# Performance work log

Measured on AMD Instinct MI355X. Metric: run time of the kernel, lower is better.

## Reference

```python
import jax, jax.numpy as jnp
import numpy as np

N_HEAD = 4
D_K = 64
D_V = 64
D_MODEL = 256
LN_EPS = 1e-5


def setup_inputs() -> dict:
    key = jax.random.key(0)
    k1, k2, k3 = jax.random.split(key, 3)
    B, C, H, W = 2, D_MODEL, 64, 64
    q = jax.random.normal(k1, (B, C, H, W), dtype=jnp.float32)
    # w_qkvs: Linear(d_model, n_head*d_k, bias=False), weight [out, in]
    std_qkv = np.sqrt(2.0 / (D_MODEL + D_K))
    w_qkv = jax.random.normal(k2, (N_HEAD * D_K, D_MODEL), dtype=jnp.float32) * std_qkv
    # fc: Linear(n_head*d_v, d_model), xavier-normal-ish init
    std_fc = np.sqrt(2.0 / (N_HEAD * D_V + D_MODEL))
    fc_w = jax.random.normal(k3, (D_MODEL, N_HEAD * D_V), dtype=jnp.float32) * std_fc
    fc_b = jnp.zeros((D_MODEL,), dtype=jnp.float32)
    ln_g = jnp.ones((D_MODEL,), dtype=jnp.float32)
    ln_b = jnp.zeros((D_MODEL,), dtype=jnp.float32)
    return {"q": q, "w_qkv": w_qkv, "fc_w": fc_w, "fc_b": fc_b, "ln_g": ln_g, "ln_b": ln_b}


def reference(q, w_qkv, fc_w, fc_b, ln_g, ln_b):
    B, C, H, W = q.shape
    L = H * W
    # [B, C, H, W] -> [B, L, C]
    x = q.reshape(B, C, L).transpose(0, 2, 1)
    residual = x
    # shared QKV projection (self-attention branch: q == k == v)
    qkv = x @ w_qkv.T                                  # [B, L, nh*dk]
    qh = qkv.reshape(B, L, N_HEAD, D_K).transpose(2, 0, 1, 3)  # [h, B, L, dk]
    scale = jnp.asarray(np.sqrt(D_K), dtype=q.dtype)
    attn = jnp.einsum('hbqd,hbkd->hbqk', qh, qh) / scale       # [h, B, L, L]
    attn = jax.nn.softmax(attn, axis=-1)
    out = jnp.einsum('hbqk,hbkd->hbqd', attn, qh)              # [h, B, L, dv]
    # [h, B, L, dv] -> [B, L, h*dv]
    out = out.transpose(1, 2, 0, 3).reshape(B, L, N_HEAD * D_V)
    out = out @ fc_w.T + fc_b
    out = out + residual
    mu = jnp.mean(out, axis=-1, keepdims=True)
    var = jnp.mean(jnp.square(out - mu), axis=-1, keepdims=True)
    out = (out - mu) / jnp.sqrt(var + LN_EPS) * ln_g + ln_b
    # raw row-major view back to [B, C, H, W] (matches torch .view)
    return out.reshape(B, -1, H, W)
```

## Files before the change

kernel.cpp:

```cpp
#include <hip/hip_runtime.h>

#define L_SEQ 4096
#define DMODEL 256
#define DH 64
#define NKB 16

typedef __attribute__((ext_vector_type(8))) __bf16 bf16x8;
typedef __attribute__((ext_vector_type(4))) float f32x4;
typedef __attribute__((ext_vector_type(16))) float f32x16;
typedef __attribute__((ext_vector_type(8))) unsigned short ushort8v;
typedef __attribute__((ext_vector_type(4))) unsigned short ushort4v;
typedef __attribute__((ext_vector_type(2))) unsigned int uint2v;
typedef __attribute__((ext_vector_type(4))) unsigned int uint4v;

__device__ __forceinline__ unsigned short f2bf(float f) {
  unsigned u = __builtin_bit_cast(unsigned, f);
  u += 0x7fffu + ((u >> 16) & 1u);
  return (unsigned short)(u >> 16);
}
__device__ __forceinline__ float bf2f(unsigned short h) {
  unsigned u = ((unsigned)h) << 16;
  return __builtin_bit_cast(float, u);
}
__device__ __forceinline__ bf16x8 ld_frag(const unsigned short* p) {
  return __builtin_bit_cast(bf16x8, *(const ushort8v*)p);
}
__device__ __forceinline__ unsigned cvtpk(float lo, float hi) {
  unsigned r;
  asm("v_cvt_pk_bf16_f32 %0, %1, %2" : "=v"(r) : "v"(lo), "v"(hi));
  return r;
}
__device__ __forceinline__ void plswap(unsigned& a, unsigned& b) {
  asm("v_permlane32_swap_b32 %0, %1" : "+v"(a), "+v"(b));
}

__global__ __launch_bounds__(256) void k_transpose(const float* __restrict__ q,
                                                   unsigned short* __restrict__ xbf,
                                                   const float* __restrict__ w,
                                                   const float* __restrict__ fcw,
                                                   unsigned short* __restrict__ wbf,
                                                   unsigned short* __restrict__ fcwbf) {
  int bx = blockIdx.x;
  int t = threadIdx.x;
  if (bx >= 512) {
    int i = ((bx - 512) * 256 + t) * 4;
    float4 a = *(const float4*)(w + i);
    float4 b = *(const float4*)(fcw + i);
    ushort4v av = {f2bf(a.x), f2bf(a.y), f2bf(a.z), f2bf(a.w)};
    ushort4v bv = {f2bf(b.x), f2bf(b.y), f2bf(b.z), f2bf(b.w)};
    *(ushort4v*)(wbf + i) = av;
    *(ushort4v*)(fcwbf + i) = bv;
    return;
  }
  __shared__ float T[64 * 65];
  int b = bx >> 8, rest = bx & 255;
  int ct = rest >> 6, lt = rest & 63;
#pragma unroll
  for (int it = 0; it < 4; ++it) {
    int i = (t >> 4) + it * 16;
    int j0 = (t & 15) * 4;
    float4 v = *(const float4*)(q + ((size_t)(b * 256 + ct * 64 + i)) * 4096 + lt * 64 + j0);
    T[i * 65 + j0 + 0] = v.x;
    T[i * 65 + j0 + 1] = v.y;
    T[i * 65 + j0 + 2] = v.z;
    T[i * 65 + j0 + 3] = v.w;
  }
  __syncthreads();
#pragma unroll
  for (int it = 0; it < 2; ++it) {
    int l = (t >> 3) + it * 32;
    int c0 = (t & 7) * 8;
    ushort8v o;
#pragma unroll
    for (int k = 0; k < 8; ++k) o[k] = f2bf(T[(c0 + k) * 65 + l]);
    *(ushort8v*)(xbf + ((size_t)(b * 4096 + lt * 64 + l)) * 256 + ct * 64 + c0) = o;
  }
}

#define KP2 136
__global__ __launch_bounds__(256) void k_qkv(const unsigned short* __restrict__ xbf,
                                             const unsigned short* __restrict__ wbf,
                                             unsigned short* __restrict__ Qh,
                                             unsigned short* __restrict__ QhT) {
  __shared__ unsigned short As[64 * KP2];
  __shared__ unsigned short Bs[64 * KP2];
  int bx = blockIdx.x;
  int mtile = bx >> 2, h = bx & 3;
  int m0 = mtile * 64;
  int b = m0 >> 12, l0 = m0 & 4095;
  int t = threadIdx.x;
  int wv = t >> 6, lane = t & 63, g = lane >> 4, ln = lane & 15;
  f32x4 acc[4] = {};
  for (int kb = 0; kb < 2; ++kb) {
#pragma unroll
    for (int it = 0; it < 4; ++it) {
      int idx = t + it * 256;
      int row = idx >> 4;
      int c0 = (idx & 15) * 8;
      *(ushort8v*)(As + row * KP2 + c0) =
          *(const ushort8v*)(xbf + (size_t)(m0 + row) * 256 + kb * 128 + c0);
      *(ushort8v*)(Bs + row * KP2 + c0) =
          *(const ushort8v*)(wbf + (size_t)(h * 64 + row) * 256 + kb * 128 + c0);
    }
    __syncthreads();
#pragma unroll
    for (int kc = 0; kc < 4; ++kc) {
      bf16x8 a = ld_frag(As + (wv * 16 + ln) * KP2 + kc * 32 + g * 8);
#pragma unroll
      for (int tn = 0; tn < 4; ++tn) {
        bf16x8 bb = ld_frag(Bs + (tn * 16 + ln) * KP2 + kc * 32 + g * 8);
        acc[tn] = __builtin_amdgcn_mfma_f32_16x16x32_bf16(a, bb, acc[tn], 0, 0, 0);
      }
    }
    __syncthreads();
  }
  size_t pbase = (size_t)(b * 4 + h);
#pragma unroll
  for (int tn = 0; tn < 4; ++tn) {
#pragma unroll
    for (int r = 0; r < 4; ++r) {
      int lrow = wv * 16 + g * 4 + r;
      int d = tn * 16 + ln;
      unsigned short bv = f2bf(acc[tn][r]);
      As[lrow * 64 + (((d >> 3) ^ (lrow & 7)) * 8) + (d & 7)] = bv;
      Bs[d * 64 + (((lrow >> 3) ^ (d & 7)) * 8) + (lrow & 7)] = bv;
    }
  }
#pragma unroll
  for (int s = 0; s < 2; ++s) {
    int flat = s * 64 + lane;
    int lrow = wv * 16 + (flat >> 3);
    int c8 = lane & 7;
    ushort8v v = *(const ushort8v*)(As + lrow * 64 + ((c8 ^ (lrow & 7)) * 8));
    *(ushort8v*)(Qh + (pbase * L_SEQ + l0 + lrow) * DH + c8 * 8) = v;
  }
  __syncthreads();
#pragma unroll
  for (int s = 0; s < 2; ++s) {
    int flat = s * 256 + t;
    int drow = flat >> 3;
    int c8 = t & 7;
    ushort8v v = *(const ushort8v*)(Bs + drow * 64 + ((c8 ^ (drow & 7)) * 8));
    *(ushort8v*)(QhT + (pbase * DH + drow) * L_SEQ + l0 + c8 * 8) = v;
  }
}

__global__ __launch_bounds__(256, 2) void k_attn(const unsigned short* __restrict__ Qh,
                                                 const unsigned short* __restrict__ QhT,
                                                 unsigned short* __restrict__ Opart,
                                                 float* __restrict__ Lpart) {
  __shared__ unsigned short smem[4 * 4096];
  int bx = blockIdx.x;
  int p = bx & 7;
  int u = bx >> 3;
  int qsup = u & 15, ks = u >> 4;
  int t = threadIdx.x;
  int wv = t >> 6, lane = t & 63, ln = lane & 31, hi = lane >> 5;
  const unsigned short* Qp = Qh + (size_t)p * L_SEQ * DH;
  const unsigned short* QTp = QhT + (size_t)p * DH * L_SEQ;
  int q0 = qsup * 256;
  int qw = q0 + wv * 64;

  bf16x8 aQ[2][4];
#pragma unroll
  for (int qt = 0; qt < 2; ++qt)
#pragma unroll
    for (int kq = 0; kq < 4; ++kq)
      aQ[qt][kq] = ld_frag(Qp + (size_t)(qw + qt * 32 + ln) * DH + kq * 16 + hi * 8);

  f32x16 oacc[2][2] = {};
  float lacc[2] = {0.f, 0.f};

  int srow0 = t >> 3, scol = t & 7;
  int srow1 = srow0 + 32;
  int sdst0 = srow0 * 64 + ((scol ^ (srow0 & 7)) * 8);
  int sdst1 = srow1 * 64 + ((scol ^ (srow1 & 7)) * 8);

  ushort8v kreg0, kreg1, vreg0, vreg1;
  {
    int kbase = (ks * NKB) * 64;
    kreg0 = *(const ushort8v*)(Qp + (size_t)(kbase + srow0) * DH + scol * 8);
    kreg1 = *(const ushort8v*)(Qp + (size_t)(kbase + srow1) * DH + scol * 8);
    vreg0 = *(const ushort8v*)(QTp + (size_t)srow0 * L_SEQ + kbase + scol * 8);
    vreg1 = *(const ushort8v*)(QTp + (size_t)srow1 * L_SEQ + kbase + scol * 8);
  }

  for (int kb = 0; kb < NKB; ++kb) {
    unsigned short* Kc = smem + (kb & 1) * 8192;
    unsigned short* Vc = Kc + 4096;
    *(ushort8v*)(Kc + sdst0) = kreg0;
    *(ushort8v*)(Kc + sdst1) = kreg1;
    *(ushort8v*)(Vc + sdst0) = vreg0;
    *(ushort8v*)(Vc + sdst1) = vreg1;
    __syncthreads();
    if (kb + 1 < NKB) {
      int kbase = (ks * NKB + kb + 1) * 64;
      kreg0 = *(const ushort8v*)(Qp + (size_t)(kbase + srow0) * DH + scol * 8);
      kreg1 = *(const ushort8v*)(Qp + (size_t)(kbase + srow1) * DH + scol * 8);
      vreg0 = *(const ushort8v*)(QTp + (size_t)srow0 * L_SEQ + kbase + scol * 8);
      vreg1 = *(const ushort8v*)(QTp + (size_t)srow1 * L_SEQ + kbase + scol * 8);
    }
#pragma unroll
    for (int mt = 0; mt < 2; ++mt) {
      int key = mt * 32 + ln;
      bf16x8 aK[4];
#pragma unroll
      for (int kq = 0; kq < 4; ++kq)
        aK[kq] = ld_frag(Kc + key * 64 + (((kq * 2 + hi) ^ (key & 7)) * 8));
      bf16x8 pf[2][2];
#pragma unroll
      for (int qt = 0; qt < 2; ++qt) {
        f32x16 s = {};
#pragma unroll
        for (int kq = 0; kq < 4; ++kq)
          s = __builtin_amdgcn_mfma_f32_32x32x16_bf16(aK[kq], aQ[qt][kq], s, 0, 0, 0);
        float pv[16];
#pragma unroll
        for (int r = 0; r < 16; ++r) pv[r] = __expf(fmaf(s[r], 0.125f, -16.0f));
        lacc[qt] += (((pv[0] + pv[1]) + (pv[2] + pv[3])) + ((pv[4] + pv[5]) + (pv[6] + pv[7]))) +
                    (((pv[8] + pv[9]) + (pv[10] + pv[11])) + ((pv[12] + pv[13]) + (pv[14] + pv[15])));
        unsigned w0 = cvtpk(pv[0], pv[1]), w1 = cvtpk(pv[2], pv[3]);
        unsigned w2 = cvtpk(pv[4], pv[5]), w3 = cvtpk(pv[6], pv[7]);
        unsigned w4 = cvtpk(pv[8], pv[9]), w5 = cvtpk(pv[10], pv[11]);
        unsigned w6 = cvtpk(pv[12], pv[13]), w7 = cvtpk(pv[14], pv[15]);
        plswap(w0, w2);
        plswap(w1, w3);
        plswap(w4, w6);
        plswap(w5, w7);
        uint4v c0 = {w0, w1, w2, w3};
        uint4v c1 = {w4, w5, w6, w7};
        pf[qt][0] = __builtin_bit_cast(bf16x8, c0);
        pf[qt][1] = __builtin_bit_cast(bf16x8, c1);
      }
#pragma unroll
      for (int dt = 0; dt < 2; ++dt) {
        int d = dt * 32 + ln;
        bf16x8 vf[2];
#pragma unroll
        for (int c = 0; c < 2; ++c)
          vf[c] = ld_frag(Vc + d * 64 + (((mt * 4 + c * 2 + hi) ^ (d & 7)) * 8));
#pragma unroll
        for (int qt = 0; qt < 2; ++qt)
#pragma unroll
          for (int c = 0; c < 2; ++c)
            oacc[dt][qt] = __builtin_amdgcn_mfma_f32_32x32x16_bf16(vf[c], pf[qt][c], oacc[dt][qt], 0, 0, 0);
      }
    }
  }
#pragma unroll
  for (int qt = 0; qt < 2; ++qt) lacc[qt] += __shfl_xor(lacc[qt], 32, 64);
  size_t pq = (size_t)(ks * 8 + p) * L_SEQ;
  if (lane < 32) {
    __builtin_nontemporal_store(lacc[0], &Lpart[pq + qw + ln]);
    __builtin_nontemporal_store(lacc[1], &Lpart[pq + qw + 32 + ln]);
  }
#pragma unroll
  for (int dt = 0; dt < 2; ++dt)
#pragma unroll
    for (int qt = 0; qt < 2; ++qt) {
      size_t rb = (pq + qw + qt * 32 + ln) * DH + dt * 32 + hi * 4;
#pragma unroll
      for (int g8 = 0; g8 < 4; ++g8) {
        uint2v wv2 = {cvtpk(oacc[dt][qt][g8 * 4 + 0], oacc[dt][qt][g8 * 4 + 1]),
                      cvtpk(oacc[dt][qt][g8 * 4 + 2], oacc[dt][qt][g8 * 4 + 3])};
        __builtin_nontemporal_store(wv2, (uint2v*)(Opart + rb + g8 * 8));
      }
    }
}

#define CP 72
__global__ __launch_bounds__(256) void k_fc(const unsigned short* __restrict__ Opart,
                                            const float* __restrict__ Lpart,
                                            const unsigned short* __restrict__ fcwbf,
                                            const float* __restrict__ qres,
                                            const float* __restrict__ fcb,
                                            const float* __restrict__ lng,
                                            const float* __restrict__ lnb,
                                            float* __restrict__ out) {
  __shared__ unsigned short As[32 * CP];
  __shared__ unsigned short Bs[256 * CP];
  __shared__ float redS[4][32], redQ[4][32], muA[32], rsA[32];
  int bx = blockIdx.x;
  int m0 = bx * 32;
  int b = m0 >> 12, lpart = m0 & 4095;
  int t = threadIdx.x;
  int wv = t >> 6, lane = t & 63, g = lane >> 4, ln = lane & 15;
  f32x4 acc[2][4] = {};
  for (int kb = 0; kb < 4; ++kb) {
    {
      int row = t >> 3, c0 = (t & 7) * 8;
      int q = lpart + row;
      int p = b * 4 + kb;
      float lsum = __builtin_nontemporal_load(&Lpart[(size_t)(0 * 8 + p) * L_SEQ + q]) +
                   __builtin_nontemporal_load(&Lpart[(size_t)(1 * 8 + p) * L_SEQ + q]) +
                   __builtin_nontemporal_load(&Lpart[(size_t)(2 * 8 + p) * L_SEQ + q]) +
                   __builtin_nontemporal_load(&Lpart[(size_t)(3 * 8 + p) * L_SEQ + q]);
      float inv = 1.0f / lsum;
      float a8[8] = {0.f, 0.f, 0.f, 0.f, 0.f, 0.f, 0.f, 0.f};
#pragma unroll
      for (int ksp = 0; ksp < 4; ++ksp) {
        ushort8v v = __builtin_nontemporal_load(
            (const ushort8v*)(Opart + ((size_t)(ksp * 8 + p) * L_SEQ + q) * DH + c0));
#pragma unroll
        for (int j = 0; j < 8; ++j) a8[j] += bf2f(v[j]);
      }
      ushort8v o;
#pragma unroll
      for (int j = 0; j < 8; ++j) o[j] = f2bf(a8[j] * inv);
      *(ushort8v*)(As + row * CP + c0) = o;
    }
#pragma unroll
    for (int it = 0; it < 8; ++it) {
      int idx = t + it * 256;
      int row = idx >> 3, c0 = (idx & 7) * 8;
      *(ushort8v*)(Bs + row * CP + c0) =
          *(const ushort8v*)(fcwbf + (size_t)row * 256 + kb * 64 + c0);
    }
    __syncthreads();
#pragma unroll
    for (int kc = 0; kc < 2; ++kc) {
      bf16x8 a[2], bb[4];
#pragma unroll
      for (int mt = 0; mt < 2; ++mt) a[mt] = ld_frag(As + (mt * 16 + ln) * CP + kc * 32 + g * 8);
#pragma unroll
      for (int tn = 0; tn < 4; ++tn) bb[tn] = ld_frag(Bs + (wv * 64 + tn * 16 + ln) * CP + kc * 32 + g * 8);
#pragma unroll
      for (int mt = 0; mt < 2; ++mt)
#pragma unroll
        for (int tn = 0; tn < 4; ++tn)
          acc[mt][tn] = __builtin_amdgcn_mfma_f32_16x16x32_bf16(a[mt], bb[tn], acc[mt][tn], 0, 0, 0);
    }
    __syncthreads();
  }
  float fb[4], lg[4], lb[4];
#pragma unroll
  for (int tn = 0; tn < 4; ++tn) {
    int o = wv * 64 + tn * 16 + ln;
    fb[tn] = fcb[o]; lg[tn] = lng[o]; lb[tn] = lnb[o];
  }
#pragma unroll
  for (int mt = 0; mt < 2; ++mt) {
    float ps[4] = {0.f, 0.f, 0.f, 0.f}, pq2[4] = {0.f, 0.f, 0.f, 0.f};
#pragma unroll
    for (int tn = 0; tn < 4; ++tn) {
      int o = wv * 64 + tn * 16 + ln;
      float4 res = *(const float4*)(qres + ((size_t)(b * 256 + o)) * 4096 + lpart + mt * 16 + g * 4);
      float rv[4] = {res.x, res.y, res.z, res.w};
#pragma unroll
      for (int r = 0; r < 4; ++r) {
        float v = acc[mt][tn][r] + fb[tn] + rv[r];
        acc[mt][tn][r] = v;
        ps[r] += v;
        pq2[r] += v * v;
      }
    }
#pragma unroll
    for (int r = 0; r < 4; ++r) {
      float s = ps[r], q2 = pq2[r];
#pragma unroll
      for (int off = 1; off < 16; off <<= 1) {
        s += __shfl_xor(s, off, 64);
        q2 += __shfl_xor(q2, off, 64);
      }
      if (ln == 0) {
        int row = mt * 16 + g * 4 + r;
        redS[wv][row] = s;
        redQ[wv][row] = q2;
      }
    }
  }
  __syncthreads();
  if (t < 32) {
    float s = redS[0][t] + redS[1][t] + redS[2][t] + redS[3][t];
    float q2 = redQ[0][t] + redQ[1][t] + redQ[2][t] + redQ[3][t];
    float mu = s * (1.f / 256.f);
    float var = q2 * (1.f / 256.f) - mu * mu;
    muA[t] = mu;
    rsA[t] = rsqrtf(var + 1e-5f);
  }
  __syncthreads();
#pragma unroll
  for (int mt = 0; mt < 2; ++mt) {
#pragma unroll
    for (int r = 0; r < 4; ++r) {
      int row = mt * 16 + g * 4 + r;
      float mu = muA[row], rs = rsA[row];
#pragma unroll
      for (int tn = 0; tn < 4; ++tn) {
        int o = wv * 64 + tn * 16 + ln;
        out[(size_t)(m0 + row) * 256 + o] = (acc[mt][tn][r] - mu) * rs * lg[tn] + lb[tn];
      }
    }
  }
}

extern "C" void kernel_launch(void* const* d_in, const int* in_sizes, int n_in,
                              void* d_out, int out_size, void* d_ws, size_t ws_size,
                              hipStream_t stream) {
  const float* q = (const float*)d_in[0];
  const float* w_qkv = (const float*)d_in[1];
  const float* fc_w = (const float*)d_in[2];
  const float* fc_b = (const float*)d_in[3];
  const float* ln_g = (const float*)d_in[4];
  const float* ln_b = (const float*)d_in[5];
  float* out = (float*)d_out;

  unsigned short* wbf = (unsigned short*)d_ws;
  unsigned short* fcwbf = wbf + 65536;
  unsigned short* xbf = fcwbf + 65536;
  unsigned short* Qh = xbf + 2097152;
  unsigned short* QhT = Qh + 2097152;
  unsigned short* Opart = QhT + 2097152;
  float* Lpart = (float*)(Opart + 8388608);

  k_transpose<<<dim3(576), dim3(256), 0, stream>>>(q, xbf, w_qkv, fc_w, wbf, fcwbf);
  k_qkv<<<dim3(512), dim3(256), 0, stream>>>(xbf, wbf, Qh, QhT);
  k_attn<<<dim3(512), dim3(256), 0, stream>>>(Qh, QhT, Opart, Lpart);
  k_fc<<<dim3(256), dim3(256), 0, stream>>>(Opart, Lpart, fcwbf, q, fc_b, ln_g, ln_b, out);
}
```

Baseline: 151.1 us.

## Template attention on key-split count, use raw exp2, drop nontemporal stores

Measured after the change: 151.5 us. No clear change (+0.3%).

```diff
diff --git a/kernel.cpp b/kernel.cpp
--- a/kernel.cpp
+++ b/kernel.cpp
@@ -3,7 +3,6 @@
 #define L_SEQ 4096
 #define DMODEL 256
 #define DH 64
-#define NKB 16
 
 typedef __attribute__((ext_vector_type(8))) __bf16 bf16x8;
 typedef __attribute__((ext_vector_type(4))) float f32x4;
@@ -32,6 +31,11 @@
 }
 __device__ __forceinline__ void plswap(unsigned& a, unsigned& b) {
   asm("v_permlane32_swap_b32 %0, %1" : "+v"(a), "+v"(b));
+}
+__device__ __forceinline__ float exp2raw(float x) {
+  float r;
+  asm("v_exp_f32 %0, %1" : "=v"(r) : "v"(x));
+  return r;
 }
 
 __global__ __launch_bounds__(256) void k_transpose(const float* __restrict__ q,
@@ -145,10 +149,14 @@
   }
 }
 
+template <int KSN>
 __global__ __launch_bounds__(256, 2) void k_attn(const unsigned short* __restrict__ Qh,
                                                  const unsigned short* __restrict__ QhT,
                                                  unsigned short* __restrict__ Opart,
                                                  float* __restrict__ Lpart) {
+  constexpr int NKB = 64 / KSN;
+  constexpr float C1 = 0.18033688011112042f;
+  constexpr float C2 = -23.083120654223414f;
   __shared__ unsigned short smem[4 * 4096];
   int bx = blockIdx.x;
   int p = bx & 7;
@@ -216,7 +224,7 @@
           s = __builtin_amdgcn_mfma_f32_32x32x16_bf16(aK[kq], aQ[qt][kq], s, 0, 0, 0);
         float pv[16];
 #pragma unroll
-        for (int r = 0; r < 16; ++r) pv[r] = __expf(fmaf(s[r], 0.125f, -16.0f));
+        for (int r = 0; r < 16; ++r) pv[r] = exp2raw(fmaf(s[r], C1, C2));
         lacc[qt] += (((pv[0] + pv[1]) + (pv[2] + pv[3])) + ((pv[4] + pv[5]) + (pv[6] + pv[7]))) +
                     (((pv[8] + pv[9]) + (pv[10] + pv[11])) + ((pv[12] + pv[13]) + (pv[14] + pv[15])));
         unsigned w0 = cvtpk(pv[0], pv[1]), w1 = cvtpk(pv[2], pv[3]);
@@ -251,8 +259,8 @@
   for (int qt = 0; qt < 2; ++qt) lacc[qt] += __shfl_xor(lacc[qt], 32, 64);
   size_t pq = (size_t)(ks * 8 + p) * L_SEQ;
   if (lane < 32) {
-    __builtin_nontemporal_store(lacc[0], &Lpart[pq + qw + ln]);
-    __builtin_nontemporal_store(lacc[1], &Lpart[pq + qw + 32 + ln]);
+    Lpart[pq + qw + ln] = lacc[0];
+    Lpart[pq + qw + 32 + ln] = lacc[1];
   }
 #pragma unroll
   for (int dt = 0; dt < 2; ++dt)
@@ -263,12 +271,13 @@
       for (int g8 = 0; g8 < 4; ++g8) {
         uint2v wv2 = {cvtpk(oacc[dt][qt][g8 * 4 + 0], oacc[dt][qt][g8 * 4 + 1]),
                       cvtpk(oacc[dt][qt][g8 * 4 + 2], oacc[dt][qt][g8 * 4 + 3])};
-        __builtin_nontemporal_store(wv2, (uint2v*)(Opart + rb + g8 * 8));
+        *(uint2v*)(Opart + rb + g8 * 8) = wv2;
       }
     }
 }
 
 #define CP 72
+template <int KSN>
 __global__ __launch_bounds__(256) void k_fc(const unsigned short* __restrict__ Opart,
                                             const float* __restrict__ Lpart,
                                             const unsigned short* __restrict__ fcwbf,
@@ -291,16 +300,14 @@
       int row = t >> 3, c0 = (t & 7) * 8;
       int q = lpart + row;
       int p = b * 4 + kb;
-      float lsum = __builtin_nontemporal_load(&Lpart[(size_t)(0 * 8 + p) * L_SEQ + q]) +
-                   __builtin_nontemporal_load(&Lpart[(size_t)(1 * 8 + p) * L_SEQ + q]) +
-                   __builtin_nontemporal_load(&Lpart[(size_t)(2 * 8 + p) * L_SEQ + q]) +
-                   __builtin_nontemporal_load(&Lpart[(size_t)(3 * 8 + p) * L_SEQ + q]);
+      float lsum = 0.f;
+#pragma unroll
+      for (int i = 0; i < KSN; ++i) lsum += Lpart[(size_t)(i * 8 + p) * L_SEQ + q];
       float inv = 1.0f / lsum;
       float a8[8] = {0.f, 0.f, 0.f, 0.f, 0.f, 0.f, 0.f, 0.f};
 #pragma unroll
-      for (int ksp = 0; ksp < 4; ++ksp) {
-        ushort8v v = __builtin_nontemporal_load(
-            (const ushort8v*)(Opart + ((size_t)(ksp * 8 + p) * L_SEQ + q) * DH + c0));
+      for (int ksp = 0; ksp < KSN; ++ksp) {
+        ushort8v v = *(const ushort8v*)(Opart + ((size_t)(ksp * 8 + p) * L_SEQ + q) * DH + c0);
 #pragma unroll
         for (int j = 0; j < 8; ++j) a8[j] += bf2f(v[j]);
       }
@@ -407,14 +414,21 @@
 
   unsigned short* wbf = (unsigned short*)d_ws;
   unsigned short* fcwbf = wbf + 65536;
-  unsigned short* xbf = fcwbf + 65536;
-  unsigned short* Qh = xbf + 2097152;
+  unsigned short* Qh = fcwbf + 65536;
   unsigned short* QhT = Qh + 2097152;
-  unsigned short* Opart = QhT + 2097152;
-  float* Lpart = (float*)(Opart + 8388608);
-
+  unsigned short* xbf = QhT + 2097152;
+  unsigned short* Opart = xbf;
+
+  bool big = ws_size >= (size_t)43253760;
   k_transpose<<<dim3(576), dim3(256), 0, stream>>>(q, xbf, w_qkv, fc_w, wbf, fcwbf);
   k_qkv<<<dim3(512), dim3(256), 0, stream>>>(xbf, wbf, Qh, QhT);
-  k_attn<<<dim3(512), dim3(256), 0, stream>>>(Qh, QhT, Opart, Lpart);
-  k_fc<<<dim3(256), dim3(256), 0, stream>>>(Opart, Lpart, fcwbf, q, fc_b, ln_g, ln_b, out);
-}
+  if (big) {
+    float* Lpart = (float*)(Opart + (size_t)8 * 2097152);
+    k_attn<8><<<dim3(1024), dim3(256), 0, stream>>>(Qh, QhT, Opart, Lpart);
+    k_fc<8><<<dim3(256), dim3(256), 0, stream>>>(Opart, Lpart, fcwbf, q, fc_b, ln_g, ln_b, out);
+  } else {
+    float* Lpart = (float*)(Opart + (size_t)4 * 2097152);
+    k_attn<4><<<dim3(512), dim3(256), 0, stream>>>(Qh, QhT, Opart, Lpart);
+    k_fc<4><<<dim3(256), dim3(256), 0, stream>>>(Opart, Lpart, fcwbf, q, fc_b, ln_g, ln_b, out);
+  }
+}
```
